# Performance work log

Hardware: AMD Instinct MI355X
Metric: run time of the kernel (lower is better)

The kernel has to match this reference:

```python
import jax, jax.numpy as jnp
import numpy as np

GROUP_SIZES = np.array([64, 48, 56, 40, 32, 24, 16, 8])
N_GROUPS = 8
MAX_GS = 64
D_MODEL = 2048
BATCH = 8192


def setup_inputs() -> dict:
    key = jax.random.key(0)
    k1, k2, k3, k4 = jax.random.split(key, 4)
    hidden = jax.random.normal(k1, (BATCH, N_GROUPS, D_MODEL), dtype=jnp.float32)
    chosen = jax.random.randint(k2, (BATCH,), 0, N_GROUPS)
    scale = 1.0 / np.sqrt(D_MODEL)  # nn.Linear default init range
    W = jax.random.uniform(k3, (N_GROUPS, MAX_GS, D_MODEL), minval=-scale, maxval=scale, dtype=jnp.float32)
    b = jax.random.uniform(k4, (N_GROUPS, MAX_GS), minval=-scale, maxval=scale, dtype=jnp.float32)
    gs = jnp.asarray(GROUP_SIZES, dtype=jnp.int32)
    # zero-pad decoder rows beyond each group's true output size
    row_mask = jnp.arange(MAX_GS)[None, :] < gs[:, None]  # [G, MAX_GS]
    W = W * row_mask[:, :, None]
    b = b * row_mask
    return {"hidden": hidden, "chosen_group_idx": chosen, "W": W, "b": b, "group_sizes": gs}


def reference(hidden, chosen_group_idx, W, b, group_sizes):
    # hidden: [B, G, D]; chosen_group_idx: [B]; W: [G, MAX_GS, D] (zero-padded); b: [G, MAX_GS]
    # Gather each sample's chosen group slice: [B, D]
    h = jnp.take_along_axis(hidden, chosen_group_idx[:, None, None], axis=1)[:, 0, :]
    Wg = W[chosen_group_idx]  # [B, MAX_GS, D]
    bg = b[chosen_group_idx]  # [B, MAX_GS]
    preds = jnp.einsum('bd,bgd->bg', h, Wg) + bg  # [B, MAX_GS]
    valid = jnp.arange(W.shape[1])[None, :] < group_sizes[chosen_group_idx][:, None]
    preds = jnp.where(valid, preds, 0.0)  # padded slots are zero, as in the torch module
    return preds, valid
```

## Files before the change

### kernel.cpp

```cpp
#include <hip/hip_runtime.h>
#include <hip/hip_bf16.h>

#define BATCH   8192
#define NGRP    8
#define MAXGS   64
#define DMODEL  2048
#define TM      16
#define TILES   (BATCH / TM)
#define NBLK    32
#define NKK     (DMODEL / 32)
#define KC      512
#define NPH     (DMODEL / KC)
#define KKP     (KC / 32)

typedef __attribute__((ext_vector_type(8))) short  short8;
typedef __attribute__((ext_vector_type(4))) float  f32x4;

#define CNT_OFF   0
#define HIST_OFF  512
#define LISTS_OFF 4096
#define W_OFF     (LISTS_OFF + NGRP * BATCH * 4)
#define CNT_STRIDE 16

static __device__ __forceinline__ short bf(float f) {
    __hip_bfloat16 h = __float2bfloat16(f);
    return (short)__bfloat16_as_ushort(h);
}

__global__ __launch_bounds__(256) void init_hist_kernel(
    const float* __restrict__ W,
    const int* __restrict__ chosen,
    unsigned short* __restrict__ Wb2,
    int* __restrict__ hist)
{
    int blk = blockIdx.x;
    int tid = threadIdx.x;
    if (blk < 1024) {
        int e = (blk * 256 + tid) * 4;
        int g = e >> 17;
        int rem = e & ((MAXGS * DMODEL) - 1);
        int c = rem >> 11;
        int k = rem & (DMODEL - 1);
        int kk = k >> 5, j = k & 31;
        float4 w = *reinterpret_cast<const float4*>(W + e);
        ushort4 o;
        o.x = (unsigned short)bf(w.x); o.y = (unsigned short)bf(w.y);
        o.z = (unsigned short)bf(w.z); o.w = (unsigned short)bf(w.w);
        size_t dst = (((size_t)g * NKK + kk) * MAXGS + c) * 32 + j;
        *reinterpret_cast<ushort4*>(Wb2 + dst) = o;
    } else {
        int hb = blk - 1024;
        __shared__ int h[NGRP];
        if (tid < NGRP) h[tid] = 0;
        __syncthreads();
        int g = chosen[hb * 256 + tid];
        atomicAdd(&h[g], 1);
        __syncthreads();
        if (tid < NGRP) hist[hb * NGRP + tid] = h[tid];
    }
}

__global__ __launch_bounds__(256) void scatter_kernel(const int* __restrict__ chosen,
                                                      const int* __restrict__ hist,
                                                      int* __restrict__ lists,
                                                      int* __restrict__ cnt) {
    __shared__ int hloc[NBLK * NGRP];
    __shared__ int gbase[NGRP];
    __shared__ int wcnt[4][NGRP];
    __shared__ int wbase[4][NGRP];
    int tid  = threadIdx.x;
    int blk  = blockIdx.x;
    int w    = tid >> 6;
    int lane = tid & 63;

    if (tid < NBLK * NGRP) hloc[tid] = hist[tid];
    __syncthreads();
    if (tid < NGRP) {
        int s = 0;
        for (int b2 = 0; b2 < blk; ++b2) s += hloc[b2 * NGRP + tid];
        gbase[tid] = s;
        if (blk == 0) {
            int tot = 0;
            for (int b2 = 0; b2 < NBLK; ++b2) tot += hloc[b2 * NGRP + tid];
            cnt[tid * CNT_STRIDE] = tot;
        }
    }

    int b = blk * 256 + tid;
    int g = chosen[b];
    int rank = 0;
    unsigned long long below = (1ull << lane) - 1ull;
    #pragma unroll
    for (int gg = 0; gg < NGRP; ++gg) {
        unsigned long long m = __ballot(g == gg);
        if (g == gg) rank = __popcll(m & below);
        if (lane == gg) wcnt[w][gg] = __popcll(m);
    }
    __syncthreads();
    if (tid < NGRP) {
        int base = gbase[tid];
        #pragma unroll
        for (int ww = 0; ww < 4; ++ww) {
            wbase[ww][tid] = base;
            base += wcnt[ww][tid];
        }
    }
    __syncthreads();
    lists[g * BATCH + wbase[w][g] + rank] = b;
}

#define LGKM0_BAR()                                          \
    asm volatile("s_waitcnt lgkmcnt(0)" ::: "memory");       \
    __builtin_amdgcn_s_barrier();                            \
    __builtin_amdgcn_sched_barrier(0)

__global__ __launch_bounds__(512, 2) void gemm_kernel(
    const float* __restrict__ hidden,
    const float* __restrict__ bias,
    const int* __restrict__ gsizes,
    const int* __restrict__ cnt,
    const int* __restrict__ lists,
    const unsigned short* __restrict__ Wb2,
    float* __restrict__ out)
{
    int bid = blockIdx.x;
    int g = bid & (NGRP - 1);
    int t = bid >> 3;
    int c = cnt[g * CNT_STRIDE];
    int m0 = t * TM;
    if (m0 >= c) return;

    __shared__ unsigned short A[2][TM][KC];

    int tid  = threadIdx.x;
    int w    = tid >> 6;
    int lane = tid & 63;

    if (w < 4) {
        const float* src[4];
        #pragma unroll
        for (int i = 0; i < 4; ++i) {
            int m  = m0 + 4 * w + i;
            int ms = m < c ? m : c - 1;
            src[i] = hidden + ((size_t)lists[g * BATCH + ms] * NGRP + g) * DMODEL
                   + lane * 8;
        }
        #define PRODUCE(buf, ph)                                               \
            {                                                                  \
                f32x4 v0[4], v1[4];                                            \
                _Pragma("unroll")                                              \
                for (int i = 0; i < 4; ++i) {                                  \
                    v0[i] = *reinterpret_cast<const f32x4*>(src[i] + (ph) * KC);     \
                    v1[i] = *reinterpret_cast<const f32x4*>(src[i] + (ph) * KC + 4); \
                }                                                              \
                _Pragma("unroll")                                              \
                for (int i = 0; i < 4; ++i) {                                  \
                    int r = 4 * w + i;                                         \
                    int swz = ((r & 7) << 4) | ((r & 1) << 6);                 \
                    short8 o;                                                  \
                    o[0] = bf(v0[i][0]); o[1] = bf(v0[i][1]);                  \
                    o[2] = bf(v0[i][2]); o[3] = bf(v0[i][3]);                  \
                    o[4] = bf(v1[i][0]); o[5] = bf(v1[i][1]);                  \
                    o[6] = bf(v1[i][2]); o[7] = bf(v1[i][3]);                  \
                    char* ab = (char*)&A[buf][r][0];                           \
                    *reinterpret_cast<short8*>(ab + ((lane * 16) ^ swz)) = o;  \
                }                                                              \
            }
        PRODUCE(0, 0)
        LGKM0_BAR();
        #pragma unroll
        for (int ch = 0; ch < NPH; ++ch) {
            if (ch + 1 < NPH) PRODUCE((ch + 1) & 1, ch + 1)
            LGKM0_BAR();
        }
        #undef PRODUCE
    } else {
        int cw   = w - 4;
        int lrow = lane & 15;
        int kg   = lane >> 4;
        int swzr = ((lrow & 7) << 4) | ((lrow & 1) << 6);
        const unsigned short* bp =
            Wb2 + (size_t)g * NKK * MAXGS * 32 + (cw * 16 + lrow) * 32 + kg * 8;

        f32x4 acc = f32x4{0, 0, 0, 0};
        LGKM0_BAR();
        #pragma unroll
        for (int ch = 0; ch < NPH; ++ch) {
            const char* arow = (const char*)&A[ch & 1][lrow][0];
            #pragma unroll
            for (int k2 = 0; k2 < KKP; ++k2) {
                int byte = (k2 * 64 + kg * 16) ^ swzr;
                short8 af  = *reinterpret_cast<const short8*>(arow + byte);
                short8 bfr = *reinterpret_cast<const short8*>(
                    bp + (size_t)(ch * KKP + k2) * MAXGS * 32);
                acc = __builtin_amdgcn_mfma_f32_16x16x32_bf16(af, bfr, acc, 0, 0, 0);
            }
            LGKM0_BAR();
        }

        int gsz = gsizes[g];
        int n = cw * 16 + lrow;
        float bv = bias[g * MAXGS + n];
        #pragma unroll
        for (int r = 0; r < 4; ++r) {
            int m = m0 + kg * 4 + r;
            if (m < c) {
                int s = lists[g * BATCH + m];
                out[(size_t)s * MAXGS + n] = acc[r] + bv;
                out[(size_t)(BATCH + s) * MAXGS + n] = (n < gsz) ? 1.0f : 0.0f;
            }
        }
    }
}

extern "C" void kernel_launch(void* const* d_in, const int* in_sizes, int n_in,
                              void* d_out, int out_size, void* d_ws, size_t ws_size,
                              hipStream_t stream) {
    const float* hidden = (const float*)d_in[0];
    const int*   chosen = (const int*)d_in[1];
    const float* W      = (const float*)d_in[2];
    const float* bias   = (const float*)d_in[3];
    const int*   gs     = (const int*)d_in[4];
    float* out = (float*)d_out;

    char* ws = (char*)d_ws;
    int* cnt   = (int*)(ws + CNT_OFF);
    int* hist  = (int*)(ws + HIST_OFF);
    int* lists = (int*)(ws + LISTS_OFF);
    unsigned short* Wb2 = (unsigned short*)(ws + W_OFF);

    init_hist_kernel<<<dim3(1024 + NBLK), dim3(256), 0, stream>>>(W, chosen, Wb2, hist);
    scatter_kernel<<<dim3(NBLK), dim3(256), 0, stream>>>(chosen, hist, lists, cnt);
    gemm_kernel<<<dim3(NGRP * TILES), dim3(512), 0, stream>>>(
        hidden, bias, gs, cnt, lists, Wb2, out);
}
```

Baseline: 35.86 us.

## Stream hidden rows into an LDS ring via direct global-to-LDS loads

```diff
diff --git a/kernel.cpp b/kernel.cpp
--- a/kernel.cpp
+++ b/kernel.cpp
@@ -6,12 +6,13 @@
 #define MAXGS   64
 #define DMODEL  2048
 #define TM      16
-#define TILES   (BATCH / TM)
 #define NBLK    32
 #define NKK     (DMODEL / 32)
-#define KC      512
+#define KC      128
 #define NPH     (DMODEL / KC)
-#define KKP     (KC / 32)
+#define RING    8
+#define PFD     6
+#define NTHR    384
 
 typedef __attribute__((ext_vector_type(8))) short  short8;
 typedef __attribute__((ext_vector_type(4))) float  f32x4;
@@ -25,6 +26,13 @@
 static __device__ __forceinline__ short bf(float f) {
     __hip_bfloat16 h = __float2bfloat16(f);
     return (short)__bfloat16_as_ushort(h);
+}
+
+static __device__ __forceinline__ void gload_lds16(const float* src, float* lds) {
+    __builtin_amdgcn_global_load_lds(
+        (const __attribute__((address_space(1))) unsigned int*)src,
+        (__attribute__((address_space(3))) unsigned int*)lds,
+        16, 0, 0);
 }
 
 __global__ __launch_bounds__(256) void init_hist_kernel(
@@ -109,12 +117,7 @@
     lists[g * BATCH + wbase[w][g] + rank] = b;
 }
 
-#define LGKM0_BAR()                                          \
-    asm volatile("s_waitcnt lgkmcnt(0)" ::: "memory");       \
-    __builtin_amdgcn_s_barrier();                            \
-    __builtin_amdgcn_sched_barrier(0)
-
-__global__ __launch_bounds__(512, 2) void gemm_kernel(
+__global__ __launch_bounds__(NTHR, 2) void gemm_kernel(
     const float* __restrict__ hidden,
     const float* __restrict__ bias,
     const int* __restrict__ gsizes,
@@ -130,72 +133,78 @@
     int m0 = t * TM;
     if (m0 >= c) return;
 
-    __shared__ unsigned short A[2][TM][KC];
+    __shared__ float A[RING][TM][KC];
 
     int tid  = threadIdx.x;
     int w    = tid >> 6;
     int lane = tid & 63;
 
-    if (w < 4) {
-        const float* src[4];
-        #pragma unroll
-        for (int i = 0; i < 4; ++i) {
-            int m  = m0 + 4 * w + i;
-            int ms = m < c ? m : c - 1;
-            src[i] = hidden + ((size_t)lists[g * BATCH + ms] * NGRP + g) * DMODEL
-                   + lane * 8;
-        }
-        #define PRODUCE(buf, ph)                                               \
+    if (w < 2) {
+        int xsw = (lane & 31) * 16;
+        const float *hb0, *hb1, *hb2, *hb3;
+        #define MKHB(i, dst)                                                   \
             {                                                                  \
-                f32x4 v0[4], v1[4];                                            \
-                _Pragma("unroll")                                              \
-                for (int i = 0; i < 4; ++i) {                                  \
-                    v0[i] = *reinterpret_cast<const f32x4*>(src[i] + (ph) * KC);     \
-                    v1[i] = *reinterpret_cast<const f32x4*>(src[i] + (ph) * KC + 4); \
-                }                                                              \
-                _Pragma("unroll")                                              \
-                for (int i = 0; i < 4; ++i) {                                  \
-                    int r = 4 * w + i;                                         \
-                    int swz = ((r & 7) << 4) | ((r & 1) << 6);                 \
-                    short8 o;                                                  \
-                    o[0] = bf(v0[i][0]); o[1] = bf(v0[i][1]);                  \
-                    o[2] = bf(v0[i][2]); o[3] = bf(v0[i][3]);                  \
-                    o[4] = bf(v1[i][0]); o[5] = bf(v1[i][1]);                  \
-                    o[6] = bf(v1[i][2]); o[7] = bf(v1[i][3]);                  \
-                    char* ab = (char*)&A[buf][r][0];                           \
-                    *reinterpret_cast<short8*>(ab + ((lane * 16) ^ swz)) = o;  \
-                }                                                              \
-            }
-        PRODUCE(0, 0)
-        LGKM0_BAR();
+                int r  = 8 * w + 2 * (i) + (lane >> 5);                        \
+                int m  = m0 + r;                                               \
+                int ms = m < c ? m : c - 1;            \
+                dst = hidden + ((size_t)lists[g * BATCH + ms] * NGRP + g) * DMODEL \
+                      + ((xsw ^ ((r & 7) << 4)) >> 2);                         \
+            }
+        MKHB(0, hb0) MKHB(1, hb1) MKHB(2, hb2) MKHB(3, hb3)
+        #undef MKHB
+
+        #define PSTAGE(ph)                                                     \
+            {                                                                  \
+                float* dst = &A[(ph) & (RING - 1)][8 * w][0];                  \
+                gload_lds16(hb0 + (ph) * KC, dst + 0 * 2 * KC);                \
+                gload_lds16(hb1 + (ph) * KC, dst + 1 * 2 * KC);                \
+                gload_lds16(hb2 + (ph) * KC, dst + 2 * 2 * KC);                \
+                gload_lds16(hb3 + (ph) * KC, dst + 3 * 2 * KC);                \
+            }
+        #define PWAIT(n) asm volatile("s_waitcnt vmcnt(" #n ")" ::: "memory")
+        #define PBAR()   __builtin_amdgcn_s_barrier(); asm volatile("" ::: "memory")
+
+        PSTAGE(0) PSTAGE(1) PSTAGE(2) PSTAGE(3) PSTAGE(4) PSTAGE(5)
+        PWAIT(20);
+        #define PPH(ch)  PBAR(); PSTAGE((ch) + PFD) PWAIT(20);
+        PPH(0) PPH(1) PPH(2) PPH(3) PPH(4) PPH(5) PPH(6) PPH(7) PPH(8) PPH(9)
+        #undef PPH
+        PBAR(); PWAIT(16);
+        PBAR(); PWAIT(12);
+        PBAR(); PWAIT(8);
+        PBAR(); PWAIT(4);
+        PBAR(); PWAIT(0);
+        PBAR();
+        #undef PSTAGE
+        #undef PWAIT
+        #undef PBAR
+    } else {
+        int cw   = w - 2;
+        int lrow = lane & 15;
+        int kg   = lane >> 4;
+        int swzr = (lrow & 7) << 4;
+        const unsigned short* bp =
+            Wb2 + (size_t)g * NKK * MAXGS * 32 + (cw * 16 + lrow) * 32 + kg * 8;
+
+        f32x4 acc = f32x4{0, 0, 0, 0};
+
         #pragma unroll
         for (int ch = 0; ch < NPH; ++ch) {
-            if (ch + 1 < NPH) PRODUCE((ch + 1) & 1, ch + 1)
-            LGKM0_BAR();
-        }
-        #undef PRODUCE
-    } else {
-        int cw   = w - 4;
-        int lrow = lane & 15;
-        int kg   = lane >> 4;
-        int swzr = ((lrow & 7) << 4) | ((lrow & 1) << 6);
-        const unsigned short* bp =
-            Wb2 + (size_t)g * NKK * MAXGS * 32 + (cw * 16 + lrow) * 32 + kg * 8;
-
-        f32x4 acc = f32x4{0, 0, 0, 0};
-        LGKM0_BAR();
-        #pragma unroll
-        for (int ch = 0; ch < NPH; ++ch) {
-            const char* arow = (const char*)&A[ch & 1][lrow][0];
+            __builtin_amdgcn_s_barrier();
+            asm volatile("" ::: "memory");
+            const char* ab = (const char*)&A[ch & (RING - 1)][lrow][0];
             #pragma unroll
-            for (int k2 = 0; k2 < KKP; ++k2) {
-                int byte = (k2 * 64 + kg * 16) ^ swzr;
-                short8 af  = *reinterpret_cast<const short8*>(arow + byte);
+            for (int ks = 0; ks < KC / 32; ++ks) {
+                int xb = ks * 128 + kg * 32;
+                f32x4 alo = *reinterpret_cast<const f32x4*>(ab + ((xb) ^ swzr));
+                f32x4 ahi = *reinterpret_cast<const f32x4*>(ab + ((xb + 16) ^ swzr));
+                short8 af;
+                af[0] = bf(alo[0]); af[1] = bf(alo[1]); af[2] = bf(alo[2]); af[3] = bf(alo[3]);
+                af[4] = bf(ahi[0]); af[5] = bf(ahi[1]); af[6] = bf(ahi[2]); af[7] = bf(ahi[3]);
                 short8 bfr = *reinterpret_cast<const short8*>(
-                    bp + (size_t)(ch * KKP + k2) * MAXGS * 32);
+                    bp + (size_t)(ch * (KC / 32) + ks) * MAXGS * 32);
                 acc = __builtin_amdgcn_mfma_f32_16x16x32_bf16(af, bfr, acc, 0, 0, 0);
             }
-            LGKM0_BAR();
         }
 
         int gsz = gsizes[g];
@@ -231,6 +240,6 @@
 
     init_hist_kernel<<<dim3(1024 + NBLK), dim3(256), 0, stream>>>(W, chosen, Wb2, hist);
     scatter_kernel<<<dim3(NBLK), dim3(256), 0, stream>>>(chosen, hist, lists, cnt);
-    gemm_kernel<<<dim3(NGRP * TILES), dim3(512), 0, stream>>>(
+    gemm_kernel<<<dim3(NGRP * (BATCH / TM)), dim3(NTHR), 0, stream>>>(
         hidden, bias, gs, cnt, lists, Wb2, out);
 }
```

Measured after the change: 34.13 us. -4.8%, faster.
